# Kernel tuning notes

Measured on AMD Instinct MI355X. Metric: run time of the kernel, lower is better.

The kernel has to match this reference:

```python
import jax, jax.numpy as jnp
import numpy as np

ALPHA = 0.3  # LeakyReLU negative slope
NEG_INF = -1e9


def setup_inputs() -> dict:
    key = jax.random.key(0)
    k1, k2, k3, k4 = jax.random.split(key, 4)
    B, N, C_IN, C_OUT, H = 4, 2048, 128, 128, 4
    node_feats = jax.random.normal(k1, (B, N, C_IN), dtype=jnp.float32)
    # xavier_uniform with gain 1.414 for projection weight [c_out, c_in]
    limit_w = 1.414 * np.sqrt(6.0 / (C_IN + C_OUT))
    W = jax.random.uniform(k2, (C_OUT, C_IN), minval=-limit_w, maxval=limit_w, dtype=jnp.float32)
    b = jnp.zeros((C_OUT,), dtype=jnp.float32)
    c_head = C_OUT // H
    limit_a = 1.414 * np.sqrt(6.0 / (H + 2 * c_head))
    a = jax.random.uniform(k3, (H, 2 * c_head), minval=-limit_a, maxval=limit_a, dtype=jnp.float32)
    return {"node_feats": node_feats, "W": W, "b": b, "a": a}


def reference(node_feats, W, b, a):
    B, N, _ = node_feats.shape
    H, two_c = a.shape
    c = two_c // 2
    # dynamic adjacency: cosine similarity, sigmoid > 0.5  <=>  sim > 0
    nf = node_feats / jnp.maximum(jnp.linalg.norm(node_feats, axis=-1, keepdims=True), 1e-12)
    sim = jnp.einsum('bid,bjd->bij', nf, nf)            # [B,N,N]
    mask = sim > 0.0                                     # adjacency (sigmoid(sim) > 0.5)
    # projection -> per-head features [B,N,H,c]
    h = (node_feats @ W.T + b).reshape(B, N, H, c)
    # edge score a . [h_i, h_j] decomposes into left/right parts
    a_l, a_r = a[:, :c], a[:, c:]                        # [H,c] each
    s_l = jnp.einsum('bnhc,hc->bnh', h, a_l)             # [B,N,H]
    s_r = jnp.einsum('bnhc,hc->bnh', h, a_r)             # [B,N,H]
    logits = jax.nn.leaky_relu(s_l[:, :, None, :] + s_r[:, None, :, :], ALPHA)  # [B,N,N,H]
    attn = jnp.where(mask[..., None], logits, NEG_INF)
    probs = jax.nn.softmax(attn, axis=2)                 # softmax over source nodes j
    # dropout is identity in eval mode
    out = jnp.einsum('bijh,bjhc->bihc', probs, h)
    return out.reshape(B, N, -1)                         # concat heads
```

## Files before the change

kernel.cpp:

```cpp
#include <hip/hip_runtime.h>
#include <cstdint>
#include <cstddef>

typedef float v16f __attribute__((ext_vector_type(16)));
typedef short v8s  __attribute__((ext_vector_type(8)));

#define MFMA32(A,B,C) __builtin_amdgcn_mfma_f32_32x32x16_bf16((A),(B),(C),0,0,0)
#define THRU 1e-3f

__device__ __forceinline__ unsigned f2bf(float f) {
  unsigned u = __builtin_bit_cast(unsigned, f);
  u += 0x7FFFu + ((u >> 16) & 1u);
  return u >> 16;
}
__device__ __forceinline__ float bf2f(unsigned us) {
  return __builtin_bit_cast(float, us << 16);
}
__device__ __forceinline__ void gload16(const void* g, void* l) {
  __builtin_amdgcn_global_load_lds(
      (const __attribute__((address_space(1))) void*)g,
      (__attribute__((address_space(3))) void*)l, 16, 0, 0);
}

__global__ __launch_bounds__(256) void gat_prep(
    const float* __restrict__ nf, const float* __restrict__ Wm,
    const float* __restrict__ bias, const float* __restrict__ aw,
    unsigned short* __restrict__ nfh, unsigned short* __restrict__ nfm,
    unsigned short* __restrict__ vt,
    float* __restrict__ EFl, float* __restrict__ EFrp)
{
  __shared__ float xl[32][132];
  const int tid = threadIdx.x;
  const int row = tid & 31, g = tid >> 5;
  const int r0 = blockIdx.x * 32;
  const int b = r0 >> 11, n0 = r0 & 2047;
  const int d0 = g * 16;

  float x[16];
  {
    const float* xp = nf + (size_t)(r0 + row) * 128 + d0;
#pragma unroll
    for (int q = 0; q < 4; ++q) {
      float4 v = *(const float4*)(xp + 4 * q);
      x[4*q+0] = v.x; x[4*q+1] = v.y; x[4*q+2] = v.z; x[4*q+3] = v.w;
    }
  }
  {
    unsigned hu[16], mu[16];
#pragma unroll
    for (int q = 0; q < 16; ++q) {
      xl[row][d0 + q] = x[q];
      unsigned hb = f2bf(x[q]); float hf = bf2f(hb);
      unsigned mb = f2bf(x[q] - hf);
      hu[q] = hb; mu[q] = mb;
    }
    const size_t to = ((size_t)(b * 64 + (n0 >> 5)) * 8 + g) * 512 + row * 8;
    uint4 p0, p1;
    p0.x = hu[0] | (hu[1] << 16);  p0.y = hu[2] | (hu[3] << 16);
    p0.z = hu[4] | (hu[5] << 16);  p0.w = hu[6] | (hu[7] << 16);
    p1.x = hu[8] | (hu[9] << 16);  p1.y = hu[10] | (hu[11] << 16);
    p1.z = hu[12] | (hu[13] << 16); p1.w = hu[14] | (hu[15] << 16);
    *(uint4*)(nfh + to) = p0; *(uint4*)(nfh + to + 256) = p1;
    p0.x = mu[0] | (mu[1] << 16);  p0.y = mu[2] | (mu[3] << 16);
    p0.z = mu[4] | (mu[5] << 16);  p0.w = mu[6] | (mu[7] << 16);
    p1.x = mu[8] | (mu[9] << 16);  p1.y = mu[10] | (mu[11] << 16);
    p1.z = mu[12] | (mu[13] << 16); p1.w = mu[14] | (mu[15] << 16);
    *(uint4*)(nfm + to) = p0; *(uint4*)(nfm + to + 256) = p1;
  }
  __syncthreads();

  float acc[16];
  const int ob = g * 16;
#pragma unroll
  for (int o = 0; o < 16; ++o) acc[o] = bias[ob + o];
  for (int dd = 0; dd < 128; dd += 4) {
    float4 xq = *(const float4*)&xl[row][dd];
#pragma unroll
    for (int o = 0; o < 16; ++o) {
      float4 wq = *(const float4*)(Wm + (size_t)(ob + o) * 128 + dd);
      acc[o] = fmaf(xq.x, wq.x, acc[o]);
      acc[o] = fmaf(xq.y, wq.y, acc[o]);
      acc[o] = fmaf(xq.z, wq.z, acc[o]);
      acc[o] = fmaf(xq.w, wq.w, acc[o]);
    }
  }
  {
    const int f = (row >> 4) & 1, kh = (row >> 3) & 1, e = row & 7;
#pragma unroll
    for (int o = 0; o < 16; ++o) {
      const int c = ob + o, hh2 = c >> 5, cc = c & 31;
      const size_t va = (((size_t)(b * 4 + hh2) * 64 + (n0 >> 5)) * 2 + f) * 512
                        + (kh * 32 + cc) * 8 + e;
      vt[va] = (unsigned short)f2bf(acc[o]);
    }
  }

  const int hh = g >> 1, cb = (g & 1) * 16;
  float sl = 0.f, sr = 0.f;
#pragma unroll
  for (int o = 0; o < 16; ++o) {
    sl = fmaf(acc[o], aw[hh * 64 + cb + o], sl);
    sr = fmaf(acc[o], aw[hh * 64 + 32 + cb + o], sr);
  }
  sl += __shfl_xor(sl, 32, 64);
  sr += __shfl_xor(sr, 32, 64);
  if (!(g & 1)) {
    const float L2E = 1.4426950408889634f;
    float El = exp2f(sl * L2E), Fl = exp2f(sl * (0.3f * L2E));
    float Er = exp2f(sr * L2E), Fr = exp2f(sr * (0.3f * L2E));
    size_t nn = (size_t)(r0 + row);
    EFl[nn * 8 + hh]     = El;
    EFl[nn * 8 + 4 + hh] = Fl;
    EFrp[nn * 8 + (hh >> 1) * 4 + (hh & 1) * 2]     = Er;
    EFrp[nn * 8 + (hh >> 1) * 4 + (hh & 1) * 2 + 1] = Fr;
  }
}

__global__ __launch_bounds__(256) void gat_mask(
    const unsigned short* __restrict__ nfh, const unsigned short* __restrict__ nfm,
    const float* __restrict__ nf, unsigned* __restrict__ mask)
{
  const int tid = threadIdx.x, lane = tid & 63;
  const int li = lane & 31, hi = lane >> 5;
  const int blk = blockIdx.x;
  const int jb = blk & 31, t = blk >> 5;
  const int ib = t & 15, b = t >> 4;
  const int i0 = ib * 128 + (tid >> 6) * 32;
  const int j0 = jb * 64;

  const size_t lbyte = (size_t)lane * 8;
  const size_t tiB  = ((size_t)(b * 64 + (i0 >> 5)) * 8) * 512 + lbyte;
  const size_t tjA0 = ((size_t)(b * 64 + (j0 >> 5)) * 8) * 512 + lbyte;
  const size_t tjA1 = tjA0 + 4096;

  v8s BH[8], BM[8];
#pragma unroll
  for (int kc = 0; kc < 8; ++kc) {
    BH[kc] = *(const v8s*)(nfh + tiB + kc * 512);
    BM[kc] = *(const v8s*)(nfm + tiB + kc * 512);
  }

  v16f S0, S1;
#pragma unroll
  for (int r = 0; r < 16; ++r) { S0[r] = 0.f; S1[r] = 0.f; }
#pragma unroll
  for (int kc = 0; kc < 8; ++kc) {
    v8s A0h = *(const v8s*)(nfh + tjA0 + kc * 512);
    v8s A1h = *(const v8s*)(nfh + tjA1 + kc * 512);
    v8s A0m = *(const v8s*)(nfm + tjA0 + kc * 512);
    v8s A1m = *(const v8s*)(nfm + tjA1 + kc * 512);
    S0 = MFMA32(A0h, BH[kc], S0);
    S1 = MFMA32(A1h, BH[kc], S1);
    S0 = MFMA32(A0h, BM[kc], S0);
    S1 = MFMA32(A1h, BM[kc], S1);
    S0 = MFMA32(A0m, BH[kc], S0);
    S1 = MFMA32(A1m, BH[kc], S1);
  }

  unsigned u0 = 0, u1 = 0;
  float mn = 1e30f;
  const int sh = hi * 4;
#pragma unroll
  for (int r = 0; r < 16; ++r) {
    const int jlc = (r & 3) + 8 * (r >> 2);
    const unsigned bit = (1u << jlc) << sh;
    if (S0[r] > 0.f) u0 |= bit;
    if (S1[r] > 0.f) u1 |= bit;
    mn = fminf(mn, fabsf(S0[r]));
    mn = fminf(mn, fabsf(S1[r]));
  }

  if (mn < THRU) {
    const float* xi = nf + ((size_t)b * 2048 + i0 + li) * 128;
#pragma unroll
    for (int sub = 0; sub < 2; ++sub) {
#pragma unroll
      for (int r = 0; r < 16; ++r) {
        const float s = sub ? S1[r] : S0[r];
        if (fabsf(s) < THRU) {
          const int jlc = (r & 3) + 8 * (r >> 2);
          const int j = j0 + sub * 32 + jlc + 4 * hi;
          const float* xj = nf + ((size_t)b * 2048 + j) * 128;
          double a = 0.0;
          for (int k = 0; k < 128; k += 2) {
            a = fma((double)xi[k],     (double)xj[k],     a);
            a = fma((double)xi[k + 1], (double)xj[k + 1], a);
          }
          const unsigned bit = (1u << jlc) << sh;
          if (sub == 0) u0 = (a > 0.0) ? (u0 | bit) : (u0 & ~bit);
          else          u1 = (a > 0.0) ? (u1 | bit) : (u1 & ~bit);
        }
      }
    }
  }

  unsigned f0 = u0 | (unsigned)__shfl_xor((int)u0, 32, 64);
  unsigned f1 = u1 | (unsigned)__shfl_xor((int)u1, 32, 64);
  if (hi == 0) {
    mask[(size_t)(b * 64 + jb * 2)     * 2048 + i0 + li] = f0;
    mask[(size_t)(b * 64 + jb * 2 + 1) * 2048 + i0 + li] = f1;
  }
}

#define PVREG(pw, h, Va, Vb)                                                   \
  {                                                                            \
    auto q0 = __builtin_amdgcn_permlane32_swap((int)pw[0], (int)pw[2], false, false); \
    auto q1 = __builtin_amdgcn_permlane32_swap((int)pw[1], (int)pw[3], false, false); \
    auto q2 = __builtin_amdgcn_permlane32_swap((int)pw[4], (int)pw[6], false, false); \
    auto q3 = __builtin_amdgcn_permlane32_swap((int)pw[5], (int)pw[7], false, false); \
    uint4 c0, c1;                                                              \
    c0.x = (unsigned)q0[0]; c0.y = (unsigned)q1[0];                            \
    c0.z = (unsigned)q0[1]; c0.w = (unsigned)q1[1];                            \
    c1.x = (unsigned)q2[0]; c1.y = (unsigned)q3[0];                            \
    c1.z = (unsigned)q2[1]; c1.w = (unsigned)q3[1];                            \
    v8s P0 = __builtin_bit_cast(v8s, c0);                                      \
    v8s P1 = __builtin_bit_cast(v8s, c1);                                      \
    acc[h] = MFMA32(P0, (Va), acc[h]);                                         \
    acc[h] = MFMA32(P1, (Vb), acc[h]);                                         \
  }

template<int CH>
__global__ __launch_bounds__(256, 2) void gat_attn(
    const unsigned short* __restrict__ vt, const float* __restrict__ EFl,
    const float* __restrict__ EFrp, const unsigned* __restrict__ mask,
    float* __restrict__ nump, float* __restrict__ denp)
{
  constexpr int JPC = 2048 / CH;
  constexpr int NT = JPC >> 5;
  __shared__ __align__(16) char sm[JPC * 16];

  const int tid = threadIdx.x, lane = tid & 63, wv = tid >> 6;
  const int li = lane & 31, hi = lane >> 5;

  const int blk = blockIdx.x;
  const int x = blk & 7, y = blk >> 3;
  const int ig = y & 15;
  const int combo = x * CH + (y >> 4);
  const int hp2 = combo & 1;
  const int r2 = combo >> 1;
  const int ch = r2 % CH, b = r2 / CH;

  const size_t nb = (size_t)b * 2048;
  const int i0 = ig * 128 + wv * 32;
  const int j0 = ch * JPC;

  float EL[2], FL[2];
  {
    const float* p = EFl + (nb + i0 + li) * 8 + 2 * hp2;
    float2 e = *(const float2*)p;
    float2 f = *(const float2*)(p + 4);
    EL[0] = e.x; EL[1] = e.y; FL[0] = f.x; FL[1] = f.y;
  }

  unsigned mw[NT];
#pragma unroll
  for (int q = 0; q < NT; ++q)
    mw[q] = mask[(size_t)(b * 64 + (j0 >> 5) + q) * 2048 + i0 + li] >> (hi * 4);

  for (int q = tid; q < JPC; q += 256)
    gload16((const char*)EFrp + (size_t)(nb + j0 + q) * 32 + (hp2 << 4),
            sm + q * 16);

  v16f acc[2];
#pragma unroll
  for (int h = 0; h < 2; ++h)
#pragma unroll
    for (int r = 0; r < 16; ++r) acc[h][r] = 0.f;
  float den[2] = {0.f, 0.f};

  const unsigned short* vb0 =
      vt + ((size_t)(b * 4 + 2 * hp2) * 64 + (j0 >> 5)) * 1024 + (size_t)lane * 8;
  const unsigned short* vb1 = vb0 + 65536;

  __syncthreads();

#pragma unroll 2
  for (int it2 = 0; it2 < NT; ++it2) {
    const unsigned mh = mw[it2];
    v8s V00 = *(const v8s*)(vb0 + it2 * 1024);
    v8s V01 = *(const v8s*)(vb0 + it2 * 1024 + 512);
    v8s V10 = *(const v8s*)(vb1 + it2 * 1024);
    v8s V11 = *(const v8s*)(vb1 + it2 * 1024 + 512);
    const char* Eb = sm + (it2 << 9);
    unsigned pA[8], pB[8];
#pragma unroll
    for (int rp = 0; rp < 8; ++rp) {
      const int r0 = 2 * rp;
      const int jl0c = (r0 & 3) + 8 * (r0 >> 2);
      const int nA = (jl0c + 4 * hi) * 16;
      float4 e0 = *(const float4*)(Eb + nA);
      float4 e1 = *(const float4*)(Eb + nA + 16);
      const bool m0 = (mh >> jl0c) & 1;
      const bool m1 = (mh >> (jl0c + 1)) & 1;
      float wA0 = fmaxf(e0.x * EL[0], e0.y * FL[0]); wA0 = m0 ? wA0 : 0.f;
      float wB0 = fmaxf(e0.z * EL[1], e0.w * FL[1]); wB0 = m0 ? wB0 : 0.f;
      float wA1 = fmaxf(e1.x * EL[0], e1.y * FL[0]); wA1 = m1 ? wA1 : 0.f;
      float wB1 = fmaxf(e1.z * EL[1], e1.w * FL[1]); wB1 = m1 ? wB1 : 0.f;
      den[0] += wA0 + wA1;
      den[1] += wB0 + wB1;
      asm("v_cvt_pk_bf16_f32 %0, %1, %2" : "=v"(pA[rp]) : "v"(wA0), "v"(wA1));
      asm("v_cvt_pk_bf16_f32 %0, %1, %2" : "=v"(pB[rp]) : "v"(wB0), "v"(wB1));
    }
    PVREG(pA, 0, V00, V01)
    PVREG(pB, 1, V10, V11)
  }

#pragma unroll
  for (int h = 0; h < 2; ++h) den[h] += __shfl_xor(den[h], 32, 64);

  const size_t obase = ((size_t)b * CH + ch) * 2048 + i0;
#pragma unroll
  for (int h = 0; h < 2; ++h) {
#pragma unroll
    for (int r = 0; r < 16; ++r) {
      const int il = (r & 3) + 8 * (r >> 2) + 4 * hi;
      nump[(obase + il) * 128 + (hp2 * 2 + h) * 32 + li] = acc[h][r];
    }
  }
  if (lane < 32) {
    float2 dv; dv.x = den[0]; dv.y = den[1];
    *(float2*)(denp + (obase + li) * 4 + 2 * hp2) = dv;
  }
}

__global__ __launch_bounds__(256) void gat_reduce(
    const float* __restrict__ nump, const float* __restrict__ denp,
    float* __restrict__ out, const int CH)
{
  const int t = blockIdx.x * 256 + threadIdx.x;
  const int b = t >> 16;
  const int rem = t & 65535;
  const int n = rem >> 5;
  const int col = (rem & 31) * 4;
  const int h = col >> 5;
  float4 s = make_float4(0.f, 0.f, 0.f, 0.f);
  float d = 0.f;
  for (int ch = 0; ch < CH; ++ch) {
    const size_t rb = ((size_t)b * CH + ch) * 2048 + n;
    float4 v = *(const float4*)(nump + rb * 128 + col);
    s.x += v.x; s.y += v.y; s.z += v.z; s.w += v.w;
    d += denp[rb * 4 + h];
  }
  float4 o;
  o.x = s.x / d; o.y = s.y / d; o.z = s.z / d; o.w = s.w / d;
  *(float4*)(out + (size_t)t * 4) = o;
}

extern "C" void kernel_launch(void* const* d_in, const int* in_sizes, int n_in,
                              void* d_out, int out_size, void* d_ws, size_t ws_size,
                              hipStream_t stream) {
  const float* nf   = (const float*)d_in[0];
  const float* Wm   = (const float*)d_in[1];
  const float* bias = (const float*)d_in[2];
  const float* aw   = (const float*)d_in[3];
  float* out = (float*)d_out;
  char* ws = (char*)d_ws;

  unsigned short* nfh  = (unsigned short*)(ws);
  unsigned short* nfm  = (unsigned short*)(ws + 2097152);
  unsigned short* vt   = (unsigned short*)(ws + 4194304);
  float*    EFl  = (float*)(ws + 6291456);
  float*    EFrp = (float*)(ws + 6553600);
  unsigned* mask = (unsigned*)(ws + 6815744);
  const size_t o_den = 8912896;

  int CH = 8;
  if (ws_size < o_den + 8ull * 4325376ull) CH = 4;

  float* denp = (float*)(ws + o_den);
  float* nump = (float*)(ws + o_den + (size_t)CH * 131072);

  gat_prep<<<256, 256, 0, stream>>>(nf, Wm, bias, aw, nfh, nfm, vt, EFl, EFrp);
  gat_mask<<<2048, 256, 0, stream>>>(nfh, nfm, nf, mask);
  if (CH == 8)
    gat_attn<8><<<1024, 256, 0, stream>>>(vt, EFl, EFrp, mask, nump, denp);
  else
    gat_attn<4><<<512, 256, 0, stream>>>(vt, EFl, EFrp, mask, nump, denp);
  gat_reduce<<<1024, 256, 0, stream>>>(nump, denp, out, CH);
}
```

Measured before the change: 76.87 us.

## Exploit symmetric similarity: compute upper-triangle mask tiles and transpose bits

The cosine-similarity adjacency is symmetric, so the mask kernel now launches only upper-triangular block pairs (1088 instead of 2048 blocks) and writes each computed 32x32 bit tile twice: directly, and transposed via a shuffle-based bit-matrix transpose. This roughly halves the MFMA similarity work and the fp64 near-threshold recomputation in the mask pass. In exchange it adds the shuffle transpose, a loop to decode the triangular block index, and divergent early exits for waves below the diagonal.

Result: faster. 70.62 us, median of 2 (-8.1%).

```diff
diff --git a/kernel.cpp b/kernel.cpp
--- a/kernel.cpp
+++ b/kernel.cpp
@@ -20,6 +20,22 @@
   __builtin_amdgcn_global_load_lds(
       (const __attribute__((address_space(1))) void*)g,
       (__attribute__((address_space(3))) void*)l, 16, 0, 0);
+}
+
+__device__ __forceinline__ unsigned btr32(unsigned x, int lane) {
+  const unsigned mj[5] = {0x0000FFFFu, 0x00FF00FFu, 0x0F0F0F0Fu,
+                          0x33333333u, 0x55555555u};
+  const int js[5] = {16, 8, 4, 2, 1};
+#pragma unroll
+  for (int s = 0; s < 5; ++s) {
+    const int j = js[s];
+    const unsigned m = mj[s];
+    unsigned xp = (unsigned)__shfl_xor((int)x, j, 64);
+    if ((lane & j) == 0) x ^= ((x ^ (xp >> j)) & m);
+    else                 x ^= (((xp ^ (x >> j)) & m) << j);
+  }
+  x = (unsigned)__shfl_xor((int)x, 31, 64);
+  return __brev(x);
 }
 
 __global__ __launch_bounds__(256) void gat_prep(
@@ -120,13 +136,19 @@
     const unsigned short* __restrict__ nfh, const unsigned short* __restrict__ nfm,
     const float* __restrict__ nf, unsigned* __restrict__ mask)
 {
-  const int tid = threadIdx.x, lane = tid & 63;
+  const int tid = threadIdx.x, lane = tid & 63, wv = tid >> 6;
   const int li = lane & 31, hi = lane >> 5;
   const int blk = blockIdx.x;
-  const int jb = blk & 31, t = blk >> 5;
-  const int ib = t & 15, b = t >> 4;
-  const int i0 = ib * 128 + (tid >> 6) * 32;
+  const int b = blk / 272;
+  const int p = blk % 272;
+  int ib = 0;
+  while (ib < 15 && (ib + 1) * (32 - ib) <= p) ++ib;
+  const int jb = 2 * ib + (p - ib * (33 - ib));
+  const int i0 = ib * 128 + wv * 32;
   const int j0 = jb * 64;
+  const int iw = i0 >> 5;
+  const int jw0 = 2 * jb, jw1 = 2 * jb + 1;
+  if (jw1 < iw) return;
 
   const size_t lbyte = (size_t)lane * 8;
   const size_t tiB  = ((size_t)(b * 64 + (i0 >> 5)) * 8) * 512 + lbyte;
@@ -196,9 +218,18 @@
 
   unsigned f0 = u0 | (unsigned)__shfl_xor((int)u0, 32, 64);
   unsigned f1 = u1 | (unsigned)__shfl_xor((int)u1, 32, 64);
+
   if (hi == 0) {
-    mask[(size_t)(b * 64 + jb * 2)     * 2048 + i0 + li] = f0;
-    mask[(size_t)(b * 64 + jb * 2 + 1) * 2048 + i0 + li] = f1;
+    if (jw0 >= iw) mask[(size_t)(b * 64 + jw0) * 2048 + i0 + li] = f0;
+    mask[(size_t)(b * 64 + jw1) * 2048 + i0 + li] = f1;
+  }
+  if (jw0 > iw) {
+    unsigned T0 = btr32(f0, lane);
+    if (hi == 0) mask[(size_t)(b * 64 + iw) * 2048 + jw0 * 32 + li] = T0;
+  }
+  if (jw1 > iw) {
+    unsigned T1 = btr32(f1, lane);
+    if (hi == 0) mask[(size_t)(b * 64 + iw) * 2048 + jw1 * 32 + li] = T1;
   }
 }
 
@@ -371,7 +402,7 @@
   float* nump = (float*)(ws + o_den + (size_t)CH * 131072);
 
   gat_prep<<<256, 256, 0, stream>>>(nf, Wm, bias, aw, nfh, nfm, vt, EFl, EFrp);
-  gat_mask<<<2048, 256, 0, stream>>>(nfh, nfm, nf, mask);
+  gat_mask<<<1088, 256, 0, stream>>>(nfh, nfm, nf, mask);
   if (CH == 8)
     gat_attn<8><<<1024, 256, 0, stream>>>(vt, EFl, EFrp, mask, nump, denp);
   else
```
